# Kernel tuning notes

Measured on AMD Instinct MI355X. Metric: run time of the kernel, lower is better.

## Reference

```python
import jax, jax.numpy as jnp
import numpy as np

H, N, L, B = 256, 64, 8192, 16   # d_model, d_state, l_max, batch
NH = N // 2                      # complex conjugate-pair halves (S4D convention)


def setup_inputs() -> dict:
    key = jax.random.key(0)
    ks = jax.random.split(key, 8)
    x = jax.random.normal(ks[0], (L, B, H), jnp.float32)
    # dt log-uniform in [1e-3, 1e-1] as in S4
    log_dt = jax.random.uniform(ks[1], (H,), jnp.float32) * (np.log(0.1) - np.log(0.001)) + np.log(0.001)
    # S4D-Lin initialization: A = -1/2 + i*pi*n
    A_real = jnp.log(0.5) * jnp.ones((H, NH), jnp.float32)            # log(-Re A)
    A_imag = np.pi * jnp.tile(jnp.arange(NH, dtype=jnp.float32), (H, 1))
    # 2 kernel channels for bidirectional
    C_real = jax.random.normal(ks[2], (2, H, NH), jnp.float32) * (0.5 ** 0.5)
    C_imag = jax.random.normal(ks[3], (2, H, NH), jnp.float32) * (0.5 ** 0.5)
    D = jax.random.normal(ks[4], (H,), jnp.float32)
    # position-wise output linear with GLU: H -> 2H, then glu over channel dim
    W_out = jax.random.normal(ks[5], (2 * H, H), jnp.float32) / np.sqrt(H)
    b_out = jnp.zeros((2 * H,), jnp.float32)
    return dict(x=x, log_dt=log_dt, A_real=A_real, A_imag=A_imag,
                C_real=C_real, C_imag=C_imag, D=D, W_out=W_out, b_out=b_out)


def _s4d_kernel(log_dt, A_real, A_imag, C_real, C_imag, length):
    """ZOH-discretized diagonal SSM kernel via Vandermonde. Returns (2, H, length) real."""
    dt = jnp.exp(log_dt)[:, None]                      # (H, 1)
    A = -jnp.exp(A_real) + 1j * A_imag                 # (H, NH)
    C = C_real + 1j * C_imag                           # (2, H, NH)
    dtA = A * dt                                       # (H, NH)
    Cd = C * (jnp.expm1(dtA) / A)                      # discretized C, (2, H, NH)
    # Vandermonde matrix exp(dtA * l) for l in [0, length)
    V = jnp.exp(dtA[:, :, None] * jnp.arange(length, dtype=jnp.float32))  # (H, NH, length)
    K = 2.0 * jnp.einsum('chn,hnl->chl', Cd, V).real   # (2, H, length)
    return K


def reference(x, log_dt, A_real, A_imag, C_real, C_imag, D, W_out, b_out):
    u = jnp.transpose(x, (1, 2, 0))                    # (B, H, L) -- TFTest transpose [1,2,0]
    Lq = u.shape[-1]
    n = 2 * Lq
    K = _s4d_kernel(log_dt, A_real, A_imag, C_real, C_imag, Lq)  # (2, H, L)
    # bidirectional: forward kernel padded right, flipped backward kernel padded left
    k = jnp.pad(K[0], ((0, 0), (0, Lq))) + jnp.pad(K[1][:, ::-1], ((0, 0), (Lq, 0)))  # (H, 2L)
    k_f = jnp.fft.rfft(k, n=n)                         # (H, n//2+1)
    u_f = jnp.fft.rfft(u, n=n)                         # (B, H, n//2+1)
    y = jnp.fft.irfft(u_f * k_f, n=n)[..., :Lq]        # (B, H, L)
    y = y + u * D[:, None]                             # skip connection
    y = jax.nn.gelu(y)
    z = jnp.einsum('oh,bhl->bol', W_out, y) + b_out[:, None]  # (B, 2H, L)
    out = z[:, :H] * jax.nn.sigmoid(z[:, H:])          # GLU over channel dim
    return out                                         # (B, H, L)
```

## Files before the change

kernel.cpp:

```cpp
#include <hip/hip_runtime.h>
#include <hip/hip_bf16.h>
#include <math.h>

#define HH  256
#define NHD 32
#define LL  8192
#define BB  16
#define HN  (HH*NHD)
#define BH  (BB*HH)
#define LC  256
#define NG  (LL/LC)
#define NINST (BB*NG)

typedef __attribute__((ext_vector_type(8))) short short8;
typedef __attribute__((ext_vector_type(4))) float floatx4;

__device__ __forceinline__ unsigned short f2bf(float f) {
  unsigned u = __float_as_uint(f);
  unsigned r = (u + 0x7FFF + ((u >> 16) & 1)) >> 16;
  return (unsigned short)r;
}
__device__ __forceinline__ unsigned packbf2(float a, float b) {
  return (unsigned)f2bf(a) | ((unsigned)f2bf(b) << 16);
}
__device__ __forceinline__ float gelu_t(float y) {
  float y2 = y * y;
  float arg = 1.5957691216f * fmaf(0.044715f * y2, y, y);
  return y / (1.f + __expf(-arg));
}

__global__ void precomp_kernel(const float* __restrict__ log_dt,
                               const float* __restrict__ A_real,
                               const float* __restrict__ A_imag,
                               const float* __restrict__ C_real,
                               const float* __restrict__ C_imag,
                               float* __restrict__ P) {
  int i = blockIdx.x * blockDim.x + threadIdx.x;
  if (i >= HN) return;
  int h = i >> 5;
  double dt  = exp((double)log_dt[h]);
  double Are = -exp((double)A_real[i]);
  double Aim = (double)A_imag[i];
  double ar = Are * dt, ai = Aim * dt;
  double ea = exp(ar);
  double wr = ea * cos(ai), wi = ea * sin(ai);
  double em_r = wr - 1.0, em_i = wi;
  double den = Are * Are + Aim * Aim;
  double rr = (em_r * Are + em_i * Aim) / den;
  double ri = (em_i * Are - em_r * Aim) / den;
  P[0*HN + i] = (float)wr;
  P[1*HN + i] = (float)wi;
  {
    double cr = (double)C_real[i], ci = (double)C_imag[i];
    P[2*HN + i] = (float)(2.0 * (cr * rr - ci * ri));
    P[3*HN + i] = (float)(2.0 * (cr * ri + ci * rr));
  }
  {
    double cr = (double)C_real[HN + i], ci = (double)C_imag[HN + i];
    P[4*HN + i] = (float)(2.0 * (cr * rr - ci * ri));
    P[5*HN + i] = (float)(2.0 * (cr * ri + ci * rr));
  }
  {
    double arL = ar * (double)LC, aiL = ai * (double)LC;
    double eaL = exp(arL);
    P[6*HN + i] = (float)(eaL * cos(aiL));
    P[7*HN + i] = (float)(eaL * sin(aiL));
  }
  P[8*HN + i] = (float)ar;
  P[9*HN + i] = (float)ai;
}

__global__ __launch_bounds__(256) void wt_frag_kernel(const float* __restrict__ W,
                                                      unsigned short* __restrict__ Wf) {
  int og = blockIdx.x;
  #pragma unroll
  for (int i = 0; i < 2; ++i) {
    int j = i * 256 + threadIdx.x;
    int ks = j >> 6, ln = (j >> 2) & 15, lg = j & 3;
    const float* src = W + (size_t)(og * 16 + ln) * 256 + ks * 32 + lg * 8;
    short8 vv;
    #pragma unroll
    for (int e = 0; e < 8; ++e) vv[e] = (short)f2bf(src[e]);
    ((short8*)Wf)[og * 512 + j] = vv;
  }
}

__global__ __launch_bounds__(256) void kprep_kernel(const float* __restrict__ P,
                                                    float* __restrict__ Kf,
                                                    float* __restrict__ Kb) {
  int i = blockIdx.x * 256 + threadIdx.x;
  int d = i & 255, h = i >> 8;
  float fd = (float)d;
  float sf = 0.f, sb = 0.f;
  #pragma unroll 4
  for (int n = 0; n < NHD; ++n) {
    int j = h * NHD + n;
    float m  = __expf(fd * P[8*HN + j]);
    float ph = fd * P[9*HN + j];
    float cs = cosf(ph), sn = sinf(ph);
    float re = m * cs, im = m * sn;
    sf += P[2*HN + j] * re - P[3*HN + j] * im;
    sb += P[4*HN + j] * re - P[5*HN + j] * im;
  }
  Kf[i] = sf;
  Kb[i] = sb;
}

__global__ __launch_bounds__(256) void tprep_kernel(const float* __restrict__ Kf,
                                                    const float* __restrict__ Kb,
                                                    const float* __restrict__ Dv,
                                                    unsigned short* __restrict__ T) {
  int h = blockIdx.x, tt = blockIdx.y;
  const float* kf = Kf + h * 256;
  const float* kb = Kb + h * 256;
  float dh = Dv[h];
  short8* out = (short8*)T;
  #pragma unroll
  for (int i = 0; i < 2; ++i) {
    int j = i * 256 + threadIdx.x;
    int ks = j >> 6, ln = (j >> 2) & 15, lg = j & 3;
    int t = tt * 16 + ln;
    short8 vv;
    #pragma unroll
    for (int e = 0; e < 8; ++e) {
      int s = ks * 32 + lg * 8 + e;
      int d = t - s;
      float v = (d > 0) ? kf[d] : ((d < 0) ? kb[-d - 1] : (kf[0] + dh));
      vv[e] = (short)f2bf(v);
    }
    out[(size_t)(h * 16 + tt) * 512 + j] = vv;
  }
}

__global__ __launch_bounds__(256) void eprep_kernel(const float* __restrict__ P,
                                                    unsigned short* __restrict__ E) {
  int h = blockIdx.x, tt = blockIdx.y;
  int j = threadIdx.x;
  int ks = j >> 6, ln = (j >> 2) & 15, lg = j & 3;
  int t = tt * 16 + ln;
  int k0 = ks * 32 + lg * 8;
  short8 vv;
  if (k0 < 64) {
    float d = (float)(t + 1);
    #pragma unroll
    for (int q = 0; q < 4; ++q) {
      int n = (k0 >> 1) + q;
      int idx = h * NHD + n;
      float m  = __expf(d * P[8*HN + idx]);
      float ph = d * P[9*HN + idx];
      float re = m * cosf(ph), im = m * sinf(ph);
      float cr = P[2*HN + idx], ci = P[3*HN + idx];
      float zr = cr * re - ci * im;
      float zi = cr * im + ci * re;
      vv[2*q]   = (short)f2bf(zr);
      vv[2*q+1] = (short)f2bf(-zi);
    }
  } else {
    float d = (float)(LC - 1 - t);
    #pragma unroll
    for (int q = 0; q < 4; ++q) {
      int n = ((k0 - 64) >> 1) + q;
      int idx = h * NHD + n;
      float m  = __expf(d * P[8*HN + idx]);
      float ph = d * P[9*HN + idx];
      float re = m * cosf(ph), im = m * sinf(ph);
      float cr = P[4*HN + idx], ci = P[5*HN + idx];
      float zr = cr * re - ci * im;
      float zi = cr * im + ci * re;
      vv[2*q]   = (short)f2bf(zr);
      vv[2*q+1] = (short)f2bf(-zi);
    }
  }
  ((short8*)E)[(size_t)(h * 16 + tt) * 256 + j] = vv;
}

__global__ __launch_bounds__(256) void vprep_kernel(const float* __restrict__ P,
                                                    unsigned short* __restrict__ V) {
  int h = blockIdx.x, mt = blockIdx.y;
  #pragma unroll
  for (int i = 0; i < 2; ++i) {
    int j = i * 256 + threadIdx.x;
    int ks = j >> 6, ln = (j >> 2) & 15, lg = j & 3;
    int row = mt * 16 + ln;
    int dir = row >> 6, nc = row & 63;
    int n = nc >> 1, comp = nc & 1;
    int idx = h * NHD + n;
    float arn = P[8*HN + idx], ain = P[9*HN + idx];
    short8 vv;
    #pragma unroll
    for (int e = 0; e < 8; ++e) {
      int s = ks * 32 + lg * 8 + e;
      float d = (float)(dir ? s : (LC - 1 - s));
      float m = __expf(d * arn);
      float ph = d * ain;
      float v = m * (comp ? sinf(ph) : cosf(ph));
      vv[e] = (short)f2bf(v);
    }
    ((short8*)V)[(size_t)(h * 8 + mt) * 512 + j] = vv;
  }
}

__global__ __launch_bounds__(256) void transpose_kernel(const float* __restrict__ x,
                                                        unsigned short* __restrict__ UF) {
  __shared__ unsigned short tile[32][264];
  int b  = blockIdx.x;
  int lb = blockIdx.y * 32;
  int tid = threadIdx.x;
  int g = lb >> 8, ks = (lb & 255) >> 5;
  int inst = b * 32 + g, it = inst >> 4, lnw = inst & 15;
  #pragma unroll
  for (int i = 0; i < 8; ++i) {
    int idx = i * 256 + tid;
    int row = idx >> 6, c4 = idx & 63;
    float4 v = *(const float4*)(x + (size_t)(lb + row) * BH + b * 256 + c4 * 4);
    ushort4 u4v;
    u4v.x = f2bf(v.x); u4v.y = f2bf(v.y); u4v.z = f2bf(v.z); u4v.w = f2bf(v.w);
    *(ushort4*)&tile[row][c4 * 4] = u4v;
  }
  __syncthreads();
  short8* out = (short8*)UF;
  #pragma unroll
  for (int i = 0; i < 4; ++i) {
    int j = i * 256 + tid;
    int h = j >> 2, lg = j & 3;
    short8 vv;
    #pragma unroll
    for (int e = 0; e < 8; ++e) vv[e] = (short)tile[lg * 8 + e][h];
    out[(size_t)(h * 32 + it) * 512 + ks * 64 + lnw * 4 + lg] = vv;
  }
}

__device__ __forceinline__ void load_bu(const short8* __restrict__ U8, int h, int it,
                                        int ln, int lg, short8 (&Bf)[8]) {
  size_t ub = (size_t)(h * 32 + it) * 512 + ln * 4 + lg;
  #pragma unroll
  for (int ks = 0; ks < 8; ++ks) Bf[ks] = U8[ub + ks * 64];
}
__device__ __forceinline__ void load_bs(const short8* __restrict__ S8, int h, int it,
                                        int ln, int lg, short8 (&Sf)[4]) {
  size_t sb = (size_t)(h * 32 + it) * 256 + ln * 4 + lg;
  #pragma unroll
  for (int ks = 0; ks < 4; ++ks) Sf[ks] = S8[sb + ks * 64];
}

__global__ __launch_bounds__(512, 2) void sfin_mfma(const unsigned short* __restrict__ V,
                                                    const unsigned short* __restrict__ UF,
                                                    float* __restrict__ Sfin) {
  int tid = threadIdx.x, w = tid >> 6, lane = tid & 63;
  int ln = lane & 15, lg = lane >> 4;
  int h = blockIdx.x;
  const short8* U8 = (const short8*)UF;
  const short8* V8 = (const short8*)V;

  short8 Vf[8];
  size_t vb = (size_t)(h * 8 + w) * 512 + ln * 4 + lg;
  #pragma unroll
  for (int ks = 0; ks < 8; ++ks) Vf[ks] = V8[vb + ks * 64];

  short8 BfA[8], BfB[8];
  load_bu(U8, h, 0, ln, lg, BfA);

  for (int it = 0; it < 32; it += 2) {
    load_bu(U8, h, it + 1, ln, lg, BfB);
    {
      floatx4 acc = (floatx4){0.f, 0.f, 0.f, 0.f};
      #pragma unroll
      for (int ks = 0; ks < 8; ++ks)
        acc = __builtin_amdgcn_mfma_f32_16x16x32_bf16(Vf[ks], BfA[ks], acc, 0, 0, 0);
      float* sp = Sfin + ((size_t)h * NINST + it * 16 + ln) * 128 + w * 16 + lg * 4;
      *(float4*)sp = (float4){acc[0], acc[1], acc[2], acc[3]};
    }
    if (it + 2 < 32) load_bu(U8, h, it + 2, ln, lg, BfA);
    {
      floatx4 acc = (floatx4){0.f, 0.f, 0.f, 0.f};
      #pragma unroll
      for (int ks = 0; ks < 8; ++ks)
        acc = __builtin_amdgcn_mfma_f32_16x16x32_bf16(Vf[ks], BfB[ks], acc, 0, 0, 0);
      float* sp = Sfin + ((size_t)h * NINST + (it + 1) * 16 + ln) * 128 + w * 16 + lg * 4;
      *(float4*)sp = (float4){acc[0], acc[1], acc[2], acc[3]};
    }
  }
}

__global__ __launch_bounds__(256) void scanB_kernel(const float* __restrict__ P,
                                                    const float* __restrict__ Sfin,
                                                    unsigned short* __restrict__ Sc) {
  int t = blockIdx.x * 256 + threadIdx.x;
  if (t >= BH * NHD) return;
  int n = t & 31, h = (t >> 5) & 255, b = t >> 13;
  float wlr = P[6*HN + h*NHD + n], wli = P[7*HN + h*NHD + n];
  unsigned* sc = (unsigned*)Sc;
  {
    int k = 2 * n;
    int ks = k >> 5, lg = (k & 31) >> 3, eh = (k & 7) >> 1;
    float ar = 0.f, ai = 0.f;
    for (int g = 0; g < NG; ++g) {
      int inst = b * NG + g;
      int it = inst >> 4, ln = inst & 15;
      size_t chunk = (size_t)(h * 32 + it) * 256 + ks * 64 + ln * 4 + lg;
      sc[chunk * 4 + eh] = packbf2(ar, ai);
      const float* sp = Sfin + ((size_t)h * NINST + inst) * 128 + 2 * n;
      float lr = sp[0], li = sp[1];
      float nr = lr + wlr * ar - wli * ai;
      float ni = li + wlr * ai + wli * ar;
      ar = nr; ai = ni;
    }
  }
  {
    int k = 64 + 2 * n;
    int ks = k >> 5, lg = (k & 31) >> 3, eh = (k & 7) >> 1;
    float ar = 0.f, ai = 0.f;
    for (int g = NG - 1; g >= 0; --g) {
      int inst = b * NG + g;
      int it = inst >> 4, ln = inst & 15;
      size_t chunk = (size_t)(h * 32 + it) * 256 + ks * 64 + ln * 4 + lg;
      sc[chunk * 4 + eh] = packbf2(ar, ai);
      const float* sp = Sfin + ((size_t)h * NINST + inst) * 128 + 64 + 2 * n;
      float lr = sp[0], li = sp[1];
      float nr = lr + wlr * ar - wli * ai;
      float ni = li + wlr * ai + wli * ar;
      ar = nr; ai = ni;
    }
  }
}

__device__ __forceinline__ void comp_y(const short8 (&Tf)[2][8], const short8 (&Ef)[2][4],
                                       const short8 (&Bf)[8], const short8 (&Sf)[4],
                                       int h, int it, int w, int ln, int lg,
                                       unsigned short* __restrict__ Y2) {
  int inst = it * 16 + ln, bb = inst >> 5, g = inst & 31;
  unsigned short* yrow = Y2 + (size_t)(bb * 256 + h) * LL + g * 256;
  #pragma unroll
  for (int t2 = 0; t2 < 2; ++t2) {
    int tt = w * 2 + t2;
    floatx4 acc = (floatx4){0.f, 0.f, 0.f, 0.f};
    #pragma unroll
    for (int ks = 0; ks < 8; ++ks)
      acc = __builtin_amdgcn_mfma_f32_16x16x32_bf16(Tf[t2][ks], Bf[ks], acc, 0, 0, 0);
    #pragma unroll
    for (int ks = 0; ks < 4; ++ks)
      acc = __builtin_amdgcn_mfma_f32_16x16x32_bf16(Ef[t2][ks], Sf[ks], acc, 0, 0, 0);
    float y0 = gelu_t(acc[0]), y1 = gelu_t(acc[1]);
    float y2v = gelu_t(acc[2]), y3 = gelu_t(acc[3]);
    uint2 vv; vv.x = packbf2(y0, y1); vv.y = packbf2(y2v, y3);
    *(uint2*)(yrow + tt * 16 + lg * 4) = vv;
  }
}

__global__ __launch_bounds__(512, 2) void yloc_corr(const unsigned short* __restrict__ T,
                                                    const unsigned short* __restrict__ E,
                                                    const unsigned short* __restrict__ Sc,
                                                    const unsigned short* __restrict__ UF,
                                                    unsigned short* __restrict__ Y2) {
  int tid = threadIdx.x, w = tid >> 6, lane = tid & 63;
  int ln = lane & 15, lg = lane >> 4;
  int h = blockIdx.x;
  const short8* T8 = (const short8*)T;
  const short8* E8 = (const short8*)E;
  const short8* S8 = (const short8*)Sc;
  const short8* U8 = (const short8*)UF;

  short8 Tf[2][8], Ef[2][4];
  #pragma unroll
  for (int t2 = 0; t2 < 2; ++t2) {
    int tt = w * 2 + t2;
    size_t tb = (size_t)(h * 16 + tt) * 512 + ln * 4 + lg;
    #pragma unroll
    for (int ks = 0; ks < 8; ++ks) Tf[t2][ks] = T8[tb + ks * 64];
    size_t eb = (size_t)(h * 16 + tt) * 256 + ln * 4 + lg;
    #pragma unroll
    for (int ks = 0; ks < 4; ++ks) Ef[t2][ks] = E8[eb + ks * 64];
  }

  short8 BfA[8], SfA[4], BfB[8], SfB[4];
  load_bu(U8, h, 0, ln, lg, BfA);
  load_bs(S8, h, 0, ln, lg, SfA);

  for (int it = 0; it < 32; it += 2) {
    load_bu(U8, h, it + 1, ln, lg, BfB);
    load_bs(S8, h, it + 1, ln, lg, SfB);
    comp_y(Tf, Ef, BfA, SfA, h, it, w, ln, lg, Y2);
    if (it + 2 < 32) {
      load_bu(U8, h, it + 2, ln, lg, BfA);
      load_bs(S8, h, it + 2, ln, lg, SfA);
    }
    comp_y(Tf, Ef, BfB, SfB, h, it + 1, w, ln, lg, Y2);
  }
}

#define RAW_W 258
__global__ __launch_bounds__(1024, 4) void gemm_mfma(
    const unsigned short* __restrict__ Wf,
    const unsigned short* __restrict__ Y2,
    const float* __restrict__ bvec, float* __restrict__ out) {
  __shared__ __align__(16) unsigned short ldsB[32768];
  __shared__ unsigned short raw[64 * RAW_W];
  int tid  = threadIdx.x;
  int w    = tid >> 6;
  int lane = tid & 63;
  int ln = lane & 15, lg = lane >> 4;
  int b  = blockIdx.x >> 6;
  int l0 = (blockIdx.x & 63) << 7;

  const short8* W8 = (const short8*)Wf;

  #pragma unroll
  for (int sl = 0; sl < 2; ++sl) {
    {
      int h = tid >> 2, lc = tid & 3;
      const unsigned short* src = Y2 + (((size_t)(b * 256 + h)) << 13) + l0 + sl * 64 + lc * 16;
      short8 v0 = ((const short8*)src)[0];
      short8 v1 = ((const short8*)src)[1];
      #pragma unroll
      for (int e = 0; e < 8; ++e) raw[(lc * 16 + e) * RAW_W + h] = (unsigned short)v0[e];
      #pragma unroll
      for (int e = 0; e < 8; ++e) raw[(lc * 16 + 8 + e) * RAW_W + h] = (unsigned short)v1[e];
    }
    __syncthreads();
    {
      int c = tid & 31, lq = tid >> 5;
      #pragma unroll
      for (int s2 = 0; s2 < 2; ++s2) {
        int lpp = lq + s2 * 32;
        int l = sl * 64 + lpp;
        short8 vv;
        #pragma unroll
        for (int e = 0; e < 8; ++e) vv[e] = (short)raw[lpp * RAW_W + c * 8 + e];
        ((short8*)ldsB)[l * 32 + (c ^ (l & 7))] = vv;
      }
    }
    __syncthreads();
  }

  int mgrp = w >> 1, ngrp = w & 1;
  floatx4 acc[4][4];
  #pragma unroll
  for (int m = 0; m < 4; ++m)
    #pragma unroll
    for (int n = 0; n < 4; ++n) acc[m][n] = (floatx4){0.f, 0.f, 0.f, 0.f};

  const short8* L8 = (const short8*)ldsB;
  #pragma unroll
  for (int ks = 0; ks < 8; ++ks) {
    short8 Bf[4];
    #pragma unroll
    for (int nf = 0; nf < 4; ++nf) {
      int row = ngrp * 64 + nf * 16 + ln;
      Bf[nf] = L8[row * 32 + ((ks * 4 + lg) ^ (row & 7))];
    }
    #pragma unroll
    for (int mm = 0; mm < 4; ++mm) {
      int og = mgrp * 2 + (mm & 1) + (mm >> 1) * 16;
      short8 Af = W8[(size_t)(og * 8 + ks) * 64 + ln * 4 + lg];
      #pragma unroll
      for (int nf = 0; nf < 4; ++nf)
        acc[mm][nf] = __builtin_amdgcn_mfma_f32_16x16x32_bf16(Af, Bf[nf], acc[mm][nf], 0, 0, 0);
    }
  }

  #pragma unroll
  for (int mm = 0; mm < 2; ++mm) {
    int obase = mgrp * 32 + mm * 16 + lg * 4;
    #pragma unroll
    for (int r = 0; r < 4; ++r) {
      int o = obase + r;
      float b0 = bvec[o];
      float b1 = bvec[HH + o];
      float* op = out + ((size_t)(b * HH + o)) * LL + l0 + ngrp * 64 + ln;
      #pragma unroll
      for (int nf = 0; nf < 4; ++nf) {
        float z1 = acc[mm][nf][r] + b0;
        float z2 = acc[mm + 2][nf][r] + b1;
        op[nf * 16] = z1 / (1.f + __expf(-z2));
      }
    }
  }
}

extern "C" void kernel_launch(void* const* d_in, const int* in_sizes, int n_in,
                              void* d_out, int out_size, void* d_ws, size_t ws_size,
                              hipStream_t stream) {
  const float* x      = (const float*)d_in[0];
  const float* log_dt = (const float*)d_in[1];
  const float* A_real = (const float*)d_in[2];
  const float* A_imag = (const float*)d_in[3];
  const float* C_real = (const float*)d_in[4];
  const float* C_imag = (const float*)d_in[5];
  const float* Dv     = (const float*)d_in[6];
  const float* W      = (const float*)d_in[7];
  const float* bvec   = (const float*)d_in[8];
  float* out = (float*)d_out;

  float* Sfin = (float*)d_out + 16777216;

  char* ws = (char*)d_ws;
  float*          P  = (float*)ws;
  unsigned short* Wf = (unsigned short*)(ws + 524288);
  float*          Kf = (float*)(ws + 786432);
  float*          Kb = (float*)(ws + 1048576);
  size_t OFF_UF = (size_t)2 << 20;
  size_t OFF_T  = OFF_UF + ((size_t)256 * 32 * 512 * 16);
  size_t OFF_E  = OFF_T + ((size_t)256 * 16 * 512 * 16);
  size_t OFF_V  = OFF_E + ((size_t)256 * 16 * 256 * 16);
  size_t OFF_SC = OFF_V + ((size_t)256 * 8 * 512 * 16);
  size_t OFF_Y2 = OFF_SC + ((size_t)256 * 32 * 256 * 16);
  unsigned short* UF = (unsigned short*)(ws + OFF_UF);
  unsigned short* T  = (unsigned short*)(ws + OFF_T);
  unsigned short* E  = (unsigned short*)(ws + OFF_E);
  unsigned short* V  = (unsigned short*)(ws + OFF_V);
  unsigned short* Sc = (unsigned short*)(ws + OFF_SC);
  unsigned short* Y2 = (unsigned short*)(ws + OFF_Y2);

  precomp_kernel<<<HN / 256, 256, 0, stream>>>(log_dt, A_real, A_imag, C_real, C_imag, P);
  wt_frag_kernel<<<32, 256, 0, stream>>>(W, Wf);
  kprep_kernel<<<HH * 256 / 256, 256, 0, stream>>>(P, Kf, Kb);
  tprep_kernel<<<dim3(HH, 16), 256, 0, stream>>>(Kf, Kb, Dv, T);
  eprep_kernel<<<dim3(HH, 16), 256, 0, stream>>>(P, E);
  vprep_kernel<<<dim3(HH, 8), 256, 0, stream>>>(P, V);
  transpose_kernel<<<dim3(BB, LL / 32), 256, 0, stream>>>(x, UF);
  sfin_mfma<<<HH, 512, 0, stream>>>(V, UF, Sfin);
  scanB_kernel<<<(BH * NHD) / 256, 256, 0, stream>>>(P, Sfin, Sc);
  yloc_corr<<<HH, 512, 0, stream>>>(T, E, Sc, UF, Y2);
  gemm_mfma<<<BB * (LL / 128), 1024, 0, stream>>>(Wf, Y2, bvec, out);
}
```

Baseline: 307.9 us.

## Store chunk-state partials in bf16 and halve GEMM block tile

The per-chunk state partials written by sfin_mfma are packed to bf16 instead of fp32, and scanB unpacks them. This halves that intermediate's write and read traffic, at the cost of lower precision feeding the recurrent scan. Separately, the output GEMM+GLU kernel moves from 1024-thread blocks covering 128 positions to 512-thread blocks covering 64 positions. That doubles the block count and halves shared memory per block, but each block reloads the full weight fragments, so total weight reads double.

```diff
diff --git a/kernel.cpp b/kernel.cpp
--- a/kernel.cpp
+++ b/kernel.cpp
@@ -19,6 +19,9 @@
   unsigned u = __float_as_uint(f);
   unsigned r = (u + 0x7FFF + ((u >> 16) & 1)) >> 16;
   return (unsigned short)r;
+}
+__device__ __forceinline__ float bf2f(unsigned short s) {
+  return __uint_as_float((unsigned)s << 16);
 }
 __device__ __forceinline__ unsigned packbf2(float a, float b) {
   return (unsigned)f2bf(a) | ((unsigned)f2bf(b) << 16);
@@ -245,7 +248,7 @@
 
 __global__ __launch_bounds__(512, 2) void sfin_mfma(const unsigned short* __restrict__ V,
                                                     const unsigned short* __restrict__ UF,
-                                                    float* __restrict__ Sfin) {
+                                                    unsigned short* __restrict__ Sfin) {
   int tid = threadIdx.x, w = tid >> 6, lane = tid & 63;
   int ln = lane & 15, lg = lane >> 4;
   int h = blockIdx.x;
@@ -267,8 +270,9 @@
       #pragma unroll
       for (int ks = 0; ks < 8; ++ks)
         acc = __builtin_amdgcn_mfma_f32_16x16x32_bf16(Vf[ks], BfA[ks], acc, 0, 0, 0);
-      float* sp = Sfin + ((size_t)h * NINST + it * 16 + ln) * 128 + w * 16 + lg * 4;
-      *(float4*)sp = (float4){acc[0], acc[1], acc[2], acc[3]};
+      unsigned short* sp = Sfin + ((size_t)h * NINST + it * 16 + ln) * 128 + w * 16 + lg * 4;
+      uint2 pv; pv.x = packbf2(acc[0], acc[1]); pv.y = packbf2(acc[2], acc[3]);
+      *(uint2*)sp = pv;
     }
     if (it + 2 < 32) load_bu(U8, h, it + 2, ln, lg, BfA);
     {
@@ -276,14 +280,15 @@
       #pragma unroll
       for (int ks = 0; ks < 8; ++ks)
         acc = __builtin_amdgcn_mfma_f32_16x16x32_bf16(Vf[ks], BfB[ks], acc, 0, 0, 0);
-      float* sp = Sfin + ((size_t)h * NINST + (it + 1) * 16 + ln) * 128 + w * 16 + lg * 4;
-      *(float4*)sp = (float4){acc[0], acc[1], acc[2], acc[3]};
+      unsigned short* sp = Sfin + ((size_t)h * NINST + (it + 1) * 16 + ln) * 128 + w * 16 + lg * 4;
+      uint2 pv; pv.x = packbf2(acc[0], acc[1]); pv.y = packbf2(acc[2], acc[3]);
+      *(uint2*)sp = pv;
     }
   }
 }
 
 __global__ __launch_bounds__(256) void scanB_kernel(const float* __restrict__ P,
-                                                    const float* __restrict__ Sfin,
+                                                    const unsigned short* __restrict__ Sfin,
                                                     unsigned short* __restrict__ Sc) {
   int t = blockIdx.x * 256 + threadIdx.x;
   if (t >= BH * NHD) return;
@@ -299,8 +304,8 @@
       int it = inst >> 4, ln = inst & 15;
       size_t chunk = (size_t)(h * 32 + it) * 256 + ks * 64 + ln * 4 + lg;
       sc[chunk * 4 + eh] = packbf2(ar, ai);
-      const float* sp = Sfin + ((size_t)h * NINST + inst) * 128 + 2 * n;
-      float lr = sp[0], li = sp[1];
+      const unsigned short* sp = Sfin + ((size_t)h * NINST + inst) * 128 + 2 * n;
+      float lr = bf2f(sp[0]), li = bf2f(sp[1]);
       float nr = lr + wlr * ar - wli * ai;
       float ni = li + wlr * ai + wli * ar;
       ar = nr; ai = ni;
@@ -315,8 +320,8 @@
       int it = inst >> 4, ln = inst & 15;
       size_t chunk = (size_t)(h * 32 + it) * 256 + ks * 64 + ln * 4 + lg;
       sc[chunk * 4 + eh] = packbf2(ar, ai);
-      const float* sp = Sfin + ((size_t)h * NINST + inst) * 128 + 64 + 2 * n;
-      float lr = sp[0], li = sp[1];
+      const unsigned short* sp = Sfin + ((size_t)h * NINST + inst) * 128 + 64 + 2 * n;
+      float lr = bf2f(sp[0]), li = bf2f(sp[1]);
       float nr = lr + wlr * ar - wli * ai;
       float ni = li + wlr * ai + wli * ar;
       ar = nr; ai = ni;
@@ -389,26 +394,26 @@
 }
 
 #define RAW_W 258
-__global__ __launch_bounds__(1024, 4) void gemm_mfma(
+__global__ __launch_bounds__(512, 4) void gemm_mfma(
     const unsigned short* __restrict__ Wf,
     const unsigned short* __restrict__ Y2,
     const float* __restrict__ bvec, float* __restrict__ out) {
-  __shared__ __align__(16) unsigned short ldsB[32768];
-  __shared__ unsigned short raw[64 * RAW_W];
+  __shared__ __align__(16) unsigned short ldsB[16384];
+  __shared__ unsigned short raw[32 * RAW_W];
   int tid  = threadIdx.x;
   int w    = tid >> 6;
   int lane = tid & 63;
   int ln = lane & 15, lg = lane >> 4;
-  int b  = blockIdx.x >> 6;
-  int l0 = (blockIdx.x & 63) << 7;
+  int b  = blockIdx.x >> 7;
+  int l0 = (blockIdx.x & 127) << 6;
 
   const short8* W8 = (const short8*)Wf;
 
   #pragma unroll
   for (int sl = 0; sl < 2; ++sl) {
     {
-      int h = tid >> 2, lc = tid & 3;
-      const unsigned short* src = Y2 + (((size_t)(b * 256 + h)) << 13) + l0 + sl * 64 + lc * 16;
+      int h = tid >> 1, lc = tid & 1;
+      const unsigned short* src = Y2 + (((size_t)(b * 256 + h)) << 13) + l0 + sl * 32 + lc * 16;
       short8 v0 = ((const short8*)src)[0];
       short8 v1 = ((const short8*)src)[1];
       #pragma unroll
@@ -421,8 +426,8 @@
       int c = tid & 31, lq = tid >> 5;
       #pragma unroll
       for (int s2 = 0; s2 < 2; ++s2) {
-        int lpp = lq + s2 * 32;
-        int l = sl * 64 + lpp;
+        int lpp = lq + s2 * 16;
+        int l = sl * 32 + lpp;
         short8 vv;
         #pragma unroll
         for (int e = 0; e < 8; ++e) vv[e] = (short)raw[lpp * RAW_W + c * 8 + e];
@@ -432,7 +437,6 @@
     __syncthreads();
   }
 
-  int mgrp = w >> 1, ngrp = w & 1;
   floatx4 acc[4][4];
   #pragma unroll
   for (int m = 0; m < 4; ++m)
@@ -445,12 +449,12 @@
     short8 Bf[4];
     #pragma unroll
     for (int nf = 0; nf < 4; ++nf) {
-      int row = ngrp * 64 + nf * 16 + ln;
+      int row = nf * 16 + ln;
       Bf[nf] = L8[row * 32 + ((ks * 4 + lg) ^ (row & 7))];
     }
     #pragma unroll
     for (int mm = 0; mm < 4; ++mm) {
-      int og = mgrp * 2 + (mm & 1) + (mm >> 1) * 16;
+      int og = w * 2 + (mm & 1) + (mm >> 1) * 16;
       short8 Af = W8[(size_t)(og * 8 + ks) * 64 + ln * 4 + lg];
       #pragma unroll
       for (int nf = 0; nf < 4; ++nf)
@@ -460,13 +464,13 @@
 
   #pragma unroll
   for (int mm = 0; mm < 2; ++mm) {
-    int obase = mgrp * 32 + mm * 16 + lg * 4;
+    int obase = w * 32 + mm * 16 + lg * 4;
     #pragma unroll
     for (int r = 0; r < 4; ++r) {
       int o = obase + r;
       float b0 = bvec[o];
       float b1 = bvec[HH + o];
-      float* op = out + ((size_t)(b * HH + o)) * LL + l0 + ngrp * 64 + ln;
+      float* op = out + ((size_t)(b * HH + o)) * LL + l0 + ln;
       #pragma unroll
       for (int nf = 0; nf < 4; ++nf) {
         float z1 = acc[mm][nf][r] + b0;
@@ -491,7 +495,7 @@
   const float* bvec   = (const float*)d_in[8];
   float* out = (float*)d_out;
 
-  float* Sfin = (float*)d_out + 16777216;
+  unsigned short* Sfin = (unsigned short*)d_out + 33554432;
 
   char* ws = (char*)d_ws;
   float*          P  = (float*)ws;
@@ -521,5 +525,5 @@
   sfin_mfma<<<HH, 512, 0, stream>>>(V, UF, Sfin);
   scanB_kernel<<<(BH * NHD) / 256, 256, 0, stream>>>(P, Sfin, Sc);
   yloc_corr<<<HH, 512, 0, stream>>>(T, E, Sc, UF, Y2);
-  gemm_mfma<<<BB * (LL / 128), 1024, 0, stream>>>(Wf, Y2, bvec, out);
-}
+  gemm_mfma<<<BB * (LL / 64), 512, 0, stream>>>(Wf, Y2, bvec, out);
+}
```

New measurement: 293.1 us. 1.05x faster.
